# Kernel tuning notes

Hardware: AMD Instinct MI355X
Metric: run time of the kernel (lower is better)

Reference implementation:

```python
import jax, jax.numpy as jnp
import numpy as np

B, N, ENC_DIM, D_CTX = 64, 4096, 512, 128
NEG_INF = -1e30
EPS = 1e-12  # F.normalize default eps


def setup_inputs() -> dict:
    key = jax.random.key(0)
    ks = jax.random.split(key, 5)
    # glorot-uniform-like bounds as in the custom Linear init
    bq_bound = np.sqrt(3.0 / ((ENC_DIM + D_CTX) / 2.0)).astype(np.float32)
    ba_bound = np.sqrt(3.0 / ((D_CTX + 1) / 2.0)).astype(np.float32)
    return {
        "kb": jax.random.normal(ks[0], (B, N, D_CTX), dtype=jnp.float32),
        "vecQuestions": jax.random.normal(ks[1], (B, ENC_DIM), dtype=jnp.float32),
        "imagesObjectNum": jax.random.randint(ks[2], (B,), 0, N, dtype=jnp.int64),
        "Wq": jax.random.uniform(ks[3], (D_CTX, ENC_DIM), jnp.float32, -bq_bound, bq_bound),
        "bq": jnp.zeros((D_CTX,), jnp.float32),
        "Wa": jax.random.uniform(ks[4], (1, D_CTX), jnp.float32, -ba_bound, ba_bound),
        "ba": jnp.zeros((1,), jnp.float32),
    }


def reference(kb, vecQuestions, imagesObjectNum, Wq, bq, Wa, ba):
    # proj_q: [B, d_ctx]
    proj_q = vecQuestions @ Wq.T + bq
    # hadamard interaction + L2 normalize along last dim (torch F.normalize)
    inter = kb * proj_q[:, None, :]                      # [B, N, d]
    norm = jnp.linalg.norm(inter, axis=-1, keepdims=True)
    inter = inter / jnp.maximum(norm, EPS)
    # inter2att: d_ctx -> 1, squeeze -> [B, N]
    raw_att = jnp.einsum("bnd,d->bn", inter, Wa[0]) + ba[0]
    # 1-D length mask: positions >= imagesObjectNum get -1e30
    pos = jnp.arange(N, dtype=raw_att.dtype)            # [N]
    mask = pos[None, :] >= imagesObjectNum[:, None].astype(raw_att.dtype)
    raw_att = jnp.where(mask, NEG_INF, raw_att)
    # alpha_entmax with alpha=1.0 == softmax
    att = jax.nn.softmax(raw_att, axis=-1)              # [B, N]
    # weighted sum over kb slots
    x_att = jnp.einsum("bn,bnd->bd", att, kb)           # [B, d_ctx]
    return x_att
```

## Files before the change

kernel.cpp:

```cpp
#include <hip/hip_runtime.h>
#include <math.h>

#define B 64
#define N 4096
#define D 128
#define E 512
#define CHUNKS 16
#define ROWS_PER_BLOCK (N / CHUNKS)
#define WAVES 4
#define ROWS_PER_WAVE (ROWS_PER_BLOCK / WAVES)
#define TILE 16
#define TILES (ROWS_PER_WAVE / TILE)
#define P (CHUNKS * WAVES)
#define NEG_BIG -1e30f
#define RSTRIDE 34

#define LDS_FENCE() asm volatile("s_waitcnt lgkmcnt(0)" ::: "memory")

__global__ __launch_bounds__(128) void proj_kernel(
    const float* __restrict__ vq, const float* __restrict__ Wq,
    const float* __restrict__ bq, const float* __restrict__ Wa,
    float* __restrict__ PQ, float* __restrict__ WPQ)
{
    int b = blockIdx.x;
    int d = blockIdx.y * 64 + (threadIdx.x >> 1);
    int eh = threadIdx.x & 1;
    const float4* w = (const float4*)(Wq + (size_t)d * E + eh * (E / 2));
    const float4* v = (const float4*)(vq + (size_t)b * E + eh * (E / 2));
    float s = 0.f;
    #pragma unroll 8
    for (int i = 0; i < E / 8; ++i) {
        float4 a = w[i], x = v[i];
        s += a.x * x.x + a.y * x.y + a.z * x.z + a.w * x.w;
    }
    s += __shfl_xor(s, 1);
    if (eh == 0) {
        float pq = s + bq[d];
        PQ[b * D + d] = pq;
        WPQ[b * D + d] = pq * Wa[d];
    }
}

__global__ __launch_bounds__(256) void att_partial_kernel(
    const float* __restrict__ kb, const int* __restrict__ cnt,
    const float* __restrict__ PQ, const float* __restrict__ WPQ,
    const float* __restrict__ ba,
    float* __restrict__ Mout, float* __restrict__ Lout, float* __restrict__ ACC)
{
    __shared__ float2 sP[WAVES][TILE * RSTRIDE];

    int blk = blockIdx.x;
    int b = blk / CHUNKS, c = blk % CHUNKS;
    int wave = threadIdx.x >> 6, lane = threadIdx.x & 63;
    int half = lane >> 5;
    int l5 = lane & 31;
    int rq_r = lane >> 2;
    int rq_q = lane & 3;

    float4 pq  = *(const float4*)(PQ  + b * D + l5 * 4);
    float4 wpq = *(const float4*)(WPQ + b * D + l5 * 4);
    float bav = ba[0];
    int limit = cnt[b];

    float m = -INFINITY, l = 0.f;
    float4 acc = {0.f, 0.f, 0.f, 0.f};

    int nwave = c * ROWS_PER_BLOCK + wave * ROWS_PER_WAVE;
    const float* lbase = kb + (size_t)b * N * D + (size_t)nwave * D + half * D + l5 * 4;

    float4 kv[8];
    #pragma unroll
    for (int j = 0; j < 8; ++j)
        kv[j] = *(const float4*)(lbase + (size_t)(2 * j) * D);

    #pragma unroll
    for (int t = 0; t < TILES; ++t) {
        #pragma unroll
        for (int j = 0; j < 8; ++j) {
            float4 k4 = kv[j];
            float s1 = k4.x * wpq.x + k4.y * wpq.y + k4.z * wpq.z + k4.w * wpq.w;
            float ax = k4.x * pq.x, ay = k4.y * pq.y, az = k4.z * pq.z, aw = k4.w * pq.w;
            float s2 = ax * ax + ay * ay + az * az + aw * aw;
            sP[wave][(2 * j + half) * RSTRIDE + l5] = make_float2(s1, s2);
        }

        float4 kvn[8];
        if (t + 1 < TILES) {
            #pragma unroll
            for (int j = 0; j < 8; ++j)
                kvn[j] = *(const float4*)(lbase + (size_t)((t + 1) * TILE + 2 * j) * D);
        }

        LDS_FENCE();

        const float2* rowp = &sP[wave][rq_r * RSTRIDE + rq_q * 8];
        float4 a0 = ((const float4*)rowp)[0];
        float4 a1 = ((const float4*)rowp)[1];
        float4 a2 = ((const float4*)rowp)[2];
        float4 a3 = ((const float4*)rowp)[3];
        float t1 = ((a0.x + a0.z) + (a1.x + a1.z)) + ((a2.x + a2.z) + (a3.x + a3.z));
        float t2 = ((a0.y + a0.w) + (a1.y + a1.w)) + ((a2.y + a2.w) + (a3.y + a3.w));
        t1 += __shfl_xor(t1, 1); t2 += __shfl_xor(t2, 1);
        t1 += __shfl_xor(t1, 2); t2 += __shfl_xor(t2, 2);

        int n = nwave + t * TILE + rq_r;
        float raw = t1 / fmaxf(sqrtf(t2), 1e-12f) + bav;
        raw = (n >= limit) ? NEG_BIG : raw;

        float mt = raw;
        mt = fmaxf(mt, __shfl_xor(mt, 4));
        mt = fmaxf(mt, __shfl_xor(mt, 8));
        mt = fmaxf(mt, __shfl_xor(mt, 16));
        mt = fmaxf(mt, __shfl_xor(mt, 32));
        float mnew = fmaxf(m, mt);
        float scale = __expf(m - mnew);
        float p = __expf(raw - mnew);

        float ps = p;
        ps += __shfl_xor(ps, 4);
        ps += __shfl_xor(ps, 8);
        ps += __shfl_xor(ps, 16);
        ps += __shfl_xor(ps, 32);
        l = l * scale + ps;
        m = mnew;

        acc.x *= scale; acc.y *= scale; acc.z *= scale; acc.w *= scale;
        #pragma unroll
        for (int j = 0; j < 8; ++j) {
            float pj = __shfl(p, 8 * j + 4 * half);
            acc.x += pj * kv[j].x; acc.y += pj * kv[j].y;
            acc.z += pj * kv[j].z; acc.w += pj * kv[j].w;
        }

        #pragma unroll
        for (int j = 0; j < 8; ++j) kv[j] = kvn[j];
    }

    acc.x += __shfl_xor(acc.x, 32);
    acc.y += __shfl_xor(acc.y, 32);
    acc.z += __shfl_xor(acc.z, 32);
    acc.w += __shfl_xor(acc.w, 32);

    int pid = b * P + c * WAVES + wave;
    if (lane == 0) { Mout[pid] = m; Lout[pid] = l; }
    if (half == 0)
        *(float4*)(ACC + (size_t)pid * D + l5 * 4) = acc;
}

__global__ __launch_bounds__(64) void merge_kernel(
    const float* __restrict__ Mv, const float* __restrict__ Lv,
    const float* __restrict__ ACC, float* __restrict__ out)
{
    int b = blockIdx.x, lane = threadIdx.x;
    float mi = Mv[b * P + lane];
    float li = Lv[b * P + lane];
    float mstar = mi;
    #pragma unroll
    for (int off = 32; off; off >>= 1) mstar = fmaxf(mstar, __shfl_xor(mstar, off));
    float cf = __expf(mi - mstar);
    float ls = cf * li;
    #pragma unroll
    for (int off = 32; off; off >>= 1) ls += __shfl_xor(ls, off);

    float2 num = {0.f, 0.f};
    const float2* accb = (const float2*)(ACC + (size_t)b * P * D);
    #pragma unroll 4
    for (int i = 0; i < P; ++i) {
        float cfi = __shfl(cf, i);
        float2 av = accb[(size_t)i * (D / 2) + lane];
        num.x += cfi * av.x;
        num.y += cfi * av.y;
    }
    float inv = 1.f / ls;
    *(float2*)(out + b * D + lane * 2) = make_float2(num.x * inv, num.y * inv);
}

extern "C" void kernel_launch(void* const* d_in, const int* in_sizes, int n_in,
                              void* d_out, int out_size, void* d_ws, size_t ws_size,
                              hipStream_t stream) {
    const float* kb  = (const float*)d_in[0];
    const float* vq  = (const float*)d_in[1];
    const int*   cnt = (const int*)d_in[2];
    const float* Wq  = (const float*)d_in[3];
    const float* bq  = (const float*)d_in[4];
    const float* Wa  = (const float*)d_in[5];
    const float* ba  = (const float*)d_in[6];
    float* out = (float*)d_out;

    float* ws = (float*)d_ws;
    float* PQ  = ws;
    float* WPQ = PQ + B * D;
    float* M   = WPQ + B * D;
    float* L   = M + B * P;
    float* ACC = L + B * P;

    proj_kernel<<<dim3(B, 2), 128, 0, stream>>>(vq, Wq, bq, Wa, PQ, WPQ);
    att_partial_kernel<<<B * CHUNKS, 256, 0, stream>>>(kb, cnt, PQ, WPQ, ba, M, L, ACC);
    merge_kernel<<<B, 64, 0, stream>>>(M, L, ACC, out);
}
```

Before: 217.2 us.

## Replace online-softmax running max with a fixed analytic bound on logits

```diff
diff --git a/kernel.cpp b/kernel.cpp
--- a/kernel.cpp
+++ b/kernel.cpp
@@ -45,7 +45,7 @@
     const float* __restrict__ kb, const int* __restrict__ cnt,
     const float* __restrict__ PQ, const float* __restrict__ WPQ,
     const float* __restrict__ ba,
-    float* __restrict__ Mout, float* __restrict__ Lout, float* __restrict__ ACC)
+    float* __restrict__ Lout, float* __restrict__ ACC)
 {
     __shared__ float2 sP[WAVES][TILE * RSTRIDE];
 
@@ -61,8 +61,9 @@
     float4 wpq = *(const float4*)(WPQ + b * D + l5 * 4);
     float bav = ba[0];
     int limit = cnt[b];
+    float K = bav + 2.0f;
 
-    float m = -INFINITY, l = 0.f;
+    float l = 0.f;
     float4 acc = {0.f, 0.f, 0.f, 0.f};
 
     int nwave = c * ROWS_PER_BLOCK + wave * ROWS_PER_WAVE;
@@ -104,27 +105,14 @@
         t1 += __shfl_xor(t1, 2); t2 += __shfl_xor(t2, 2);
 
         int n = nwave + t * TILE + rq_r;
-        float raw = t1 / fmaxf(sqrtf(t2), 1e-12f) + bav;
+        float inv = __builtin_amdgcn_rsqf(fmaxf(t2, 1e-24f));
+        float raw = t1 * inv + bav;
         raw = (n >= limit) ? NEG_BIG : raw;
+        if (limit == 0) raw = K;
+        float p = __expf(raw - K);
 
-        float mt = raw;
-        mt = fmaxf(mt, __shfl_xor(mt, 4));
-        mt = fmaxf(mt, __shfl_xor(mt, 8));
-        mt = fmaxf(mt, __shfl_xor(mt, 16));
-        mt = fmaxf(mt, __shfl_xor(mt, 32));
-        float mnew = fmaxf(m, mt);
-        float scale = __expf(m - mnew);
-        float p = __expf(raw - mnew);
+        l += p;
 
-        float ps = p;
-        ps += __shfl_xor(ps, 4);
-        ps += __shfl_xor(ps, 8);
-        ps += __shfl_xor(ps, 16);
-        ps += __shfl_xor(ps, 32);
-        l = l * scale + ps;
-        m = mnew;
-
-        acc.x *= scale; acc.y *= scale; acc.z *= scale; acc.w *= scale;
         #pragma unroll
         for (int j = 0; j < 8; ++j) {
             float pj = __shfl(p, 8 * j + 4 * half);
@@ -136,43 +124,36 @@
         for (int j = 0; j < 8; ++j) kv[j] = kvn[j];
     }
 
+    l += __shfl_xor(l, 4);
+    l += __shfl_xor(l, 8);
+    l += __shfl_xor(l, 16);
+    l += __shfl_xor(l, 32);
+
     acc.x += __shfl_xor(acc.x, 32);
     acc.y += __shfl_xor(acc.y, 32);
     acc.z += __shfl_xor(acc.z, 32);
     acc.w += __shfl_xor(acc.w, 32);
 
     int pid = b * P + c * WAVES + wave;
-    if (lane == 0) { Mout[pid] = m; Lout[pid] = l; }
+    if (lane == 0) Lout[pid] = l;
     if (half == 0)
         *(float4*)(ACC + (size_t)pid * D + l5 * 4) = acc;
 }
 
-__global__ __launch_bounds__(64) void merge_kernel(
-    const float* __restrict__ Mv, const float* __restrict__ Lv,
-    const float* __restrict__ ACC, float* __restrict__ out)
+__global__ __launch_bounds__(128) void merge_kernel(
+    const float* __restrict__ Lv, const float* __restrict__ ACC,
+    float* __restrict__ out)
 {
-    int b = blockIdx.x, lane = threadIdx.x;
-    float mi = Mv[b * P + lane];
-    float li = Lv[b * P + lane];
-    float mstar = mi;
-    #pragma unroll
-    for (int off = 32; off; off >>= 1) mstar = fmaxf(mstar, __shfl_xor(mstar, off));
-    float cf = __expf(mi - mstar);
-    float ls = cf * li;
-    #pragma unroll
-    for (int off = 32; off; off >>= 1) ls += __shfl_xor(ls, off);
-
-    float2 num = {0.f, 0.f};
-    const float2* accb = (const float2*)(ACC + (size_t)b * P * D);
-    #pragma unroll 4
-    for (int i = 0; i < P; ++i) {
-        float cfi = __shfl(cf, i);
-        float2 av = accb[(size_t)i * (D / 2) + lane];
-        num.x += cfi * av.x;
-        num.y += cfi * av.y;
-    }
-    float inv = 1.f / ls;
-    *(float2*)(out + b * D + lane * 2) = make_float2(num.x * inv, num.y * inv);
+    int b = blockIdx.x, d = threadIdx.x;
+    const float* Lb = Lv + b * P;
+    float lsum = 0.f;
+    #pragma unroll 8
+    for (int i = 0; i < P; ++i) lsum += Lb[i];
+    float num = 0.f;
+    const float* accb = ACC + (size_t)b * P * D + d;
+    #pragma unroll 8
+    for (int i = 0; i < P; ++i) num += accb[(size_t)i * D];
+    out[b * D + d] = num / lsum;
 }
 
 extern "C" void kernel_launch(void* const* d_in, const int* in_sizes, int n_in,
@@ -190,11 +171,10 @@
     float* ws = (float*)d_ws;
     float* PQ  = ws;
     float* WPQ = PQ + B * D;
-    float* M   = WPQ + B * D;
-    float* L   = M + B * P;
+    float* L   = WPQ + B * D;
     float* ACC = L + B * P;
 
     proj_kernel<<<dim3(B, 2), 128, 0, stream>>>(vq, Wq, bq, Wa, PQ, WPQ);
-    att_partial_kernel<<<B * CHUNKS, 256, 0, stream>>>(kb, cnt, PQ, WPQ, ba, M, L, ACC);
-    merge_kernel<<<B, 64, 0, stream>>>(M, L, ACC, out);
+    att_partial_kernel<<<B * CHUNKS, 256, 0, stream>>>(kb, cnt, PQ, WPQ, ba, L, ACC);
+    merge_kernel<<<B, 128, 0, stream>>>(L, ACC, out);
 }
```

After: 216.2 us. Within noise of the previous version (-0.4%).
